# Kernel optimization log

Hardware: AMD Instinct MI355X
Metric: run time of the kernel (lower is better)

The kernel has to match this reference:

```python
import jax, jax.numpy as jnp
import numpy as np

B, H, W, C = 8, 256, 256, 256


def setup_inputs() -> dict:
    key = jax.random.key(0)
    ks = jax.random.split(key, 5)
    scale = 1.0 / np.sqrt(C)
    return {
        "x": jax.random.normal(ks[0], (B, H, W, C), dtype=jnp.float32),
        "wq": jax.random.normal(ks[1], (C, C), dtype=jnp.float32) * scale,
        "bq": jnp.zeros((C,), dtype=jnp.float32),
        "wk": jax.random.normal(ks[2], (C, C), dtype=jnp.float32) * scale,
        "bk": jnp.zeros((C,), dtype=jnp.float32),
        "wv": jax.random.normal(ks[3], (C, C), dtype=jnp.float32) * scale,
        "bv": jnp.zeros((C,), dtype=jnp.float32),
        "gamma": jax.random.normal(ks[4], (C,), dtype=jnp.float32) * scale,
    }


def reference(x, wq, bq, wk, bk, wv, bv, gamma):
    # 1x1 convs == per-pixel channel matmuls
    q = jnp.einsum("bhwc,cd->bhwd", x, wq) + bq  # [B,H,W,C]
    k = jnp.einsum("bhwc,cd->bhwd", x, wk) + bk
    v = jnp.einsum("bhwc,cd->bhwd", x, wv) + bv
    # tf.matmul(q, k, transpose_b=True) on 4D: batch dims (B,H), attention over W
    attn = jax.nn.softmax(jnp.einsum("bhic,bhjc->bhij", q, k), axis=-1)  # [B,H,W,W]
    out = jnp.einsum("bhij,bhjc->bhic", attn, v)  # [B,H,W,C]
    return gamma * out + x
```

## Files before the change

kernel.cpp:

```cpp
#include <hip/hip_runtime.h>


#define NPAIR 2048
#define SEQ 256
#define DIM 256
#define XSTR 264
#define SCRSTR 48

typedef __attribute__((ext_vector_type(8))) short bf16x8;
typedef __attribute__((ext_vector_type(4))) float f32x4;
typedef __attribute__((ext_vector_type(4))) unsigned uint4v;
typedef __attribute__((ext_vector_type(2))) unsigned uint2v;

__device__ __forceinline__ unsigned short f2bf(float f) {
  union { float f; unsigned u; } v; v.f = f;
  unsigned r = v.u + 0x7FFFu + ((v.u >> 16) & 1u);
  return (unsigned short)(r >> 16);
}
__device__ __forceinline__ unsigned pack2(float a, float b) {
  return (unsigned)f2bf(a) | ((unsigned)f2bf(b) << 16);
}

__global__ void prep_kernel(const float* __restrict__ wq, const float* __restrict__ bq,
                            const float* __restrict__ wk, const float* __restrict__ wv,
                            unsigned short* __restrict__ MT, unsigned short* __restrict__ WvT,
                            float* __restrict__ u) {
  int b = blockIdx.x, t = threadIdx.x;
  if (b < 256) {
    int r = b;
    for (int c = t; c < 256; c += blockDim.x) {
      float acc = 0.f;
      for (int d = 0; d < 256; ++d) acc += wq[c * 256 + d] * wk[r * 256 + d];
      MT[r * 256 + c] = f2bf(acc);
    }
  } else if (b == 256) {
    for (int cc = t; cc < 256; cc += blockDim.x) {
      float acc = 0.f;
      for (int d = 0; d < 256; ++d) acc += wk[cc * 256 + d] * bq[d];
      u[cc] = acc;
    }
  } else {
    int r = b - 257;
    for (int c = t; c < 256; c += blockDim.x) WvT[r * 256 + c] = f2bf(wv[c * 256 + r]);
  }
}

__global__ __launch_bounds__(512, 2)
void attn_fused_kernel(const float* __restrict__ x, const unsigned short* __restrict__ MT,
                       const float* __restrict__ u, const unsigned short* __restrict__ WvT,
                       const float* __restrict__ bv, const float* __restrict__ gamma,
                       float* __restrict__ out) {
  __shared__ unsigned short Xs[SEQ * XSTR];
  __shared__ unsigned short Yscr[8][16 * SCRSTR];
  const int p = blockIdx.x;
  const long xbase = (long)p * (SEQ * DIM);
  const int tid = threadIdx.x;
  const int wid = tid >> 6;
  const int ln = tid & 63;
  const int l16 = ln & 15;
  const int quad = ln >> 4;

  for (int it = 0; it < 64; ++it) {
    int idx = 2 * (tid + 512 * it);
    float2 v = *(const float2*)(x + xbase + idx);
    int j = idx >> 8, c = idx & 255;
    unsigned pack = (unsigned)f2bf(v.x) | ((unsigned)f2bf(v.y) << 16);
    *(unsigned*)&Xs[j * XSTR + c] = pack;
  }
  __syncthreads();

  float ureg[16];
#pragma unroll
  for (int nt = 0; nt < 16; ++nt) ureg[nt] = u[nt * 16 + l16];

  unsigned short* Aout =
      (unsigned short*)((char*)out + (size_t)p * (SEQ * DIM * 4) + 131072);
  unsigned short* scr = &Yscr[wid][0];

  for (int ch = 0; ch < 2; ++ch) {
    const int chunk = wid + 8 * ch;
    const int i0 = chunk * 16;

    f32x4 acc[16];
#pragma unroll
    for (int nt = 0; nt < 16; ++nt) acc[nt] = (f32x4){0.f, 0.f, 0.f, 0.f};
#pragma unroll
    for (int ks = 0; ks < 8; ++ks) {
      bf16x8 a = *(const bf16x8*)&Xs[(i0 + l16) * XSTR + ks * 32 + quad * 8];
#pragma unroll
      for (int nt = 0; nt < 16; ++nt) {
        bf16x8 b = *(const bf16x8*)&MT[(nt * 16 + l16) * 256 + ks * 32 + quad * 8];
        acc[nt] = __builtin_amdgcn_mfma_f32_16x16x32_bf16(a, b, acc[nt], 0, 0, 0);
      }
    }

    f32x4 sacc[16];
#pragma unroll
    for (int mt = 0; mt < 16; ++mt) sacc[mt] = (f32x4){0.f, 0.f, 0.f, 0.f};
#pragma unroll
    for (int e = 0; e < 8; ++e) {
      asm volatile("s_waitcnt lgkmcnt(0)" ::: "memory");
#pragma unroll
      for (int h = 0; h < 2; ++h) {
        int nt = 2 * e + h;
#pragma unroll
        for (int r = 0; r < 4; ++r) {
          float yv = acc[nt][r] + ureg[nt];
          scr[(quad * 4 + r) * SCRSTR + h * 16 + l16] = f2bf(yv);
        }
      }
      asm volatile("s_waitcnt lgkmcnt(0)" ::: "memory");
      bf16x8 bfrag = *(const bf16x8*)&scr[l16 * SCRSTR + quad * 8];
#pragma unroll
      for (int mt = 0; mt < 16; ++mt) {
        bf16x8 a = *(const bf16x8*)&Xs[(mt * 16 + l16) * XSTR + e * 32 + quad * 8];
        sacc[mt] = __builtin_amdgcn_mfma_f32_16x16x32_bf16(a, bfrag, sacc[mt], 0, 0, 0);
      }
    }

    float mx = -1e30f;
#pragma unroll
    for (int mt = 0; mt < 16; ++mt)
#pragma unroll
      for (int r = 0; r < 4; ++r) mx = fmaxf(mx, sacc[mt][r]);
    mx = fmaxf(mx, __shfl_xor(mx, 16, 64));
    mx = fmaxf(mx, __shfl_xor(mx, 32, 64));
    float sum = 0.f;
#pragma unroll
    for (int mt = 0; mt < 16; ++mt)
#pragma unroll
      for (int r = 0; r < 4; ++r) {
        float ev = exp2f((sacc[mt][r] - mx) * 1.44269504088896340736f);
        sacc[mt][r] = ev;
        sum += ev;
      }
    sum += __shfl_xor(sum, 16, 64);
    sum += __shfl_xor(sum, 32, 64);
    float rs = 1.0f / sum;

#pragma unroll
    for (int ks = 0; ks < 8; ++ks) {
      asm volatile("s_waitcnt lgkmcnt(0)" ::: "memory");
#pragma unroll
      for (int h = 0; h < 2; ++h) {
        int mt = 2 * ks + h;
        unsigned lo = pack2(sacc[mt][0] * rs, sacc[mt][1] * rs);
        unsigned hi = pack2(sacc[mt][2] * rs, sacc[mt][3] * rs);
        *(unsigned*)&scr[l16 * SCRSTR + h * 16 + quad * 4] = lo;
        *(unsigned*)&scr[l16 * SCRSTR + h * 16 + quad * 4 + 2] = hi;
      }
      asm volatile("s_waitcnt lgkmcnt(0)" ::: "memory");
      uint4v t = *(const uint4v*)&scr[(ln >> 2) * SCRSTR + (ln & 3) * 8];
      *(uint4v*)&Aout[(i0 + (ln >> 2)) * 256 + ks * 32 + (ln & 3) * 8] = t;
    }
  }
  __syncthreads();

  bf16x8 afr[8];
  {
    int i = 16 * wid + l16;
#pragma unroll
    for (int ks = 0; ks < 8; ++ks)
      afr[ks] = *(const bf16x8*)&Aout[i * 256 + ks * 32 + quad * 8];
  }

  unsigned pay[64];
#pragma unroll
  for (int dc = 0; dc < 16; ++dc) {
    bf16x8 bfr[8];
#pragma unroll
    for (int ks = 0; ks < 8; ++ks)
      bfr[ks] = *(const bf16x8*)&WvT[(dc * 16 + l16) * 256 + ks * 32 + quad * 8];
#pragma unroll
    for (int jr = 0; jr < 2; ++jr) {
      const int jc = wid + 8 * jr;
      f32x4 vacc = (f32x4){0.f, 0.f, 0.f, 0.f};
#pragma unroll
      for (int ks = 0; ks < 8; ++ks) {
        bf16x8 a = *(const bf16x8*)&Xs[(jc * 16 + l16) * XSTR + ks * 32 + quad * 8];
        vacc = __builtin_amdgcn_mfma_f32_16x16x32_bf16(a, bfr[ks], vacc, 0, 0, 0);
      }
      pay[dc * 4 + jr * 2 + 0] = pack2(vacc[0], vacc[1]);
      pay[dc * 4 + jr * 2 + 1] = pack2(vacc[2], vacc[3]);
    }
  }
  __syncthreads();
#pragma unroll
  for (int dc = 0; dc < 16; ++dc)
#pragma unroll
    for (int jr = 0; jr < 2; ++jr) {
      const int jc = wid + 8 * jr;
      uint2v w = {pay[dc * 4 + jr * 2], pay[dc * 4 + jr * 2 + 1]};
      *(uint2v*)&Xs[(dc * 16 + l16) * XSTR + jc * 16 + quad * 4] = w;
    }
  float greg[16], bvreg[16];
#pragma unroll
  for (int nt = 0; nt < 16; ++nt) {
    greg[nt] = gamma[nt * 16 + l16];
    bvreg[nt] = bv[nt * 16 + l16];
  }
  __syncthreads();

  float* outp = out + (size_t)p * (SEQ * DIM);
  for (int rnd = 0; rnd < 2; ++rnd) {
    const int i0 = (wid + 8 * rnd) * 16;
    f32x4 oacc[16];
#pragma unroll
    for (int nt = 0; nt < 16; ++nt) oacc[nt] = (f32x4){0.f, 0.f, 0.f, 0.f};
#pragma unroll
    for (int ks = 0; ks < 8; ++ks) {
      bf16x8 a = afr[ks];
#pragma unroll
      for (int nt = 0; nt < 16; ++nt) {
        bf16x8 b = *(const bf16x8*)&Xs[(nt * 16 + l16) * XSTR + ks * 32 + quad * 8];
        oacc[nt] = __builtin_amdgcn_mfma_f32_16x16x32_bf16(a, b, oacc[nt], 0, 0, 0);
      }
    }
    if (rnd == 0) {
      int i = 16 * (8 + wid) + l16;
#pragma unroll
      for (int ks = 0; ks < 8; ++ks)
        afr[ks] = *(const bf16x8*)&Aout[i * 256 + ks * 32 + quad * 8];
      asm volatile("s_waitcnt vmcnt(0)" ::: "memory");
      __syncthreads();
    }
#pragma unroll
    for (int nt = 0; nt < 16; ++nt)
#pragma unroll
      for (int r = 0; r < 4; ++r) {
        int i = i0 + quad * 4 + r;
        int dd = nt * 16 + l16;
        float xv = x[xbase + (long)i * 256 + dd];
        outp[(long)i * 256 + dd] = greg[nt] * (oacc[nt][r] + bvreg[nt]) + xv;
      }
  }
}

extern "C" void kernel_launch(void* const* d_in, const int* in_sizes, int n_in,
                              void* d_out, int out_size, void* d_ws, size_t ws_size,
                              hipStream_t stream) {
  const float* x     = (const float*)d_in[0];
  const float* wq    = (const float*)d_in[1];
  const float* bq    = (const float*)d_in[2];
  const float* wk    = (const float*)d_in[3];
  const float* wv    = (const float*)d_in[5];
  const float* bv    = (const float*)d_in[6];
  const float* gamma = (const float*)d_in[7];
  float* out = (float*)d_out;

  unsigned short* MT  = (unsigned short*)d_ws;
  unsigned short* WvT = MT + 65536;
  float* u            = (float*)(WvT + 65536);

  prep_kernel<<<513, 256, 0, stream>>>(wq, bq, wk, wv, MT, WvT, u);
  attn_fused_kernel<<<NPAIR, 512, 0, stream>>>(x, MT, u, WvT, bv, gamma, out);
}
```

Baseline: 2.457 ms.

## Use 1024-thread blocks with one 16-row chunk per wave, keep attention in registers

The fused kernel now launches 16 waves per block so each wave owns exactly one 16-row query chunk, removing the two-chunk loops. Attention probabilities stay in registers and go through the per-wave scratch into the PV matmul, instead of being written as bf16 to the output buffer in global memory and read back. The V projection is computed per wave for its own rows, and the x load uses float4. The risk is register pressure under launch_bounds(1024,4): the attention values held across the V-projection stage could spill, and with about 143KB of LDS per block occupancy drops to one block per CU.

```diff
diff --git a/kernel.cpp b/kernel.cpp
--- a/kernel.cpp
+++ b/kernel.cpp
@@ -9,7 +9,6 @@
 
 typedef __attribute__((ext_vector_type(8))) short bf16x8;
 typedef __attribute__((ext_vector_type(4))) float f32x4;
-typedef __attribute__((ext_vector_type(4))) unsigned uint4v;
 typedef __attribute__((ext_vector_type(2))) unsigned uint2v;
 
 __device__ __forceinline__ unsigned short f2bf(float f) {
@@ -45,13 +44,13 @@
   }
 }
 
-__global__ __launch_bounds__(512, 2)
+__global__ __launch_bounds__(1024, 4)
 void attn_fused_kernel(const float* __restrict__ x, const unsigned short* __restrict__ MT,
                        const float* __restrict__ u, const unsigned short* __restrict__ WvT,
                        const float* __restrict__ bv, const float* __restrict__ gamma,
                        float* __restrict__ out) {
   __shared__ unsigned short Xs[SEQ * XSTR];
-  __shared__ unsigned short Yscr[8][16 * SCRSTR];
+  __shared__ unsigned short Yscr[16][16 * SCRSTR];
   const int p = blockIdx.x;
   const long xbase = (long)p * (SEQ * DIM);
   const int tid = threadIdx.x;
@@ -59,13 +58,14 @@
   const int ln = tid & 63;
   const int l16 = ln & 15;
   const int quad = ln >> 4;
-
-  for (int it = 0; it < 64; ++it) {
-    int idx = 2 * (tid + 512 * it);
-    float2 v = *(const float2*)(x + xbase + idx);
+  const int i0 = wid * 16;
+
+  for (int it = 0; it < 16; ++it) {
+    int idx = 4 * (tid + 1024 * it);
+    float4 v = *(const float4*)(x + xbase + idx);
     int j = idx >> 8, c = idx & 255;
-    unsigned pack = (unsigned)f2bf(v.x) | ((unsigned)f2bf(v.y) << 16);
-    *(unsigned*)&Xs[j * XSTR + c] = pack;
+    uint2v w = {pack2(v.x, v.y), pack2(v.z, v.w)};
+    *(uint2v*)&Xs[j * XSTR + c] = w;
   }
   __syncthreads();
 
@@ -73,126 +73,95 @@
 #pragma unroll
   for (int nt = 0; nt < 16; ++nt) ureg[nt] = u[nt * 16 + l16];
 
-  unsigned short* Aout =
-      (unsigned short*)((char*)out + (size_t)p * (SEQ * DIM * 4) + 131072);
   unsigned short* scr = &Yscr[wid][0];
 
-  for (int ch = 0; ch < 2; ++ch) {
-    const int chunk = wid + 8 * ch;
-    const int i0 = chunk * 16;
-
-    f32x4 acc[16];
-#pragma unroll
-    for (int nt = 0; nt < 16; ++nt) acc[nt] = (f32x4){0.f, 0.f, 0.f, 0.f};
+  f32x4 acc[16];
+#pragma unroll
+  for (int nt = 0; nt < 16; ++nt) acc[nt] = (f32x4){0.f, 0.f, 0.f, 0.f};
+#pragma unroll
+  for (int ks = 0; ks < 8; ++ks) {
+    bf16x8 a = *(const bf16x8*)&Xs[(i0 + l16) * XSTR + ks * 32 + quad * 8];
+#pragma unroll
+    for (int nt = 0; nt < 16; ++nt) {
+      bf16x8 b = *(const bf16x8*)&MT[(nt * 16 + l16) * 256 + ks * 32 + quad * 8];
+      acc[nt] = __builtin_amdgcn_mfma_f32_16x16x32_bf16(a, b, acc[nt], 0, 0, 0);
+    }
+  }
+
+  f32x4 sacc[16];
+#pragma unroll
+  for (int mt = 0; mt < 16; ++mt) sacc[mt] = (f32x4){0.f, 0.f, 0.f, 0.f};
+#pragma unroll
+  for (int e = 0; e < 8; ++e) {
+    asm volatile("s_waitcnt lgkmcnt(0)" ::: "memory");
+#pragma unroll
+    for (int h = 0; h < 2; ++h) {
+      int nt = 2 * e + h;
+#pragma unroll
+      for (int r = 0; r < 4; ++r) {
+        float yv = acc[nt][r] + ureg[nt];
+        scr[(quad * 4 + r) * SCRSTR + h * 16 + l16] = f2bf(yv);
+      }
+    }
+    asm volatile("s_waitcnt lgkmcnt(0)" ::: "memory");
+    bf16x8 bfrag = *(const bf16x8*)&scr[l16 * SCRSTR + quad * 8];
+#pragma unroll
+    for (int mt = 0; mt < 16; ++mt) {
+      bf16x8 a = *(const bf16x8*)&Xs[(mt * 16 + l16) * XSTR + e * 32 + quad * 8];
+      sacc[mt] = __builtin_amdgcn_mfma_f32_16x16x32_bf16(a, bfrag, sacc[mt], 0, 0, 0);
+    }
+  }
+
+  float mx = -1e30f;
+#pragma unroll
+  for (int mt = 0; mt < 16; ++mt)
+#pragma unroll
+    for (int r = 0; r < 4; ++r) mx = fmaxf(mx, sacc[mt][r]);
+  mx = fmaxf(mx, __shfl_xor(mx, 16, 64));
+  mx = fmaxf(mx, __shfl_xor(mx, 32, 64));
+  float sum = 0.f;
+#pragma unroll
+  for (int mt = 0; mt < 16; ++mt)
+#pragma unroll
+    for (int r = 0; r < 4; ++r) {
+      float ev = exp2f((sacc[mt][r] - mx) * 1.44269504088896340736f);
+      sacc[mt][r] = ev;
+      sum += ev;
+    }
+  sum += __shfl_xor(sum, 16, 64);
+  sum += __shfl_xor(sum, 32, 64);
+  float rs = 1.0f / sum;
+
+  unsigned aw[32];
+#pragma unroll
+  for (int mt = 0; mt < 16; ++mt) {
+    aw[2 * mt]     = pack2(sacc[mt][0] * rs, sacc[mt][1] * rs);
+    aw[2 * mt + 1] = pack2(sacc[mt][2] * rs, sacc[mt][3] * rs);
+  }
+
+  bf16x8 axr[8];
+#pragma unroll
+  for (int ks = 0; ks < 8; ++ks)
+    axr[ks] = *(const bf16x8*)&Xs[(i0 + l16) * XSTR + ks * 32 + quad * 8];
+  unsigned pay[32];
+#pragma unroll
+  for (int dc = 0; dc < 16; ++dc) {
+    f32x4 vacc = (f32x4){0.f, 0.f, 0.f, 0.f};
 #pragma unroll
     for (int ks = 0; ks < 8; ++ks) {
-      bf16x8 a = *(const bf16x8*)&Xs[(i0 + l16) * XSTR + ks * 32 + quad * 8];
-#pragma unroll
-      for (int nt = 0; nt < 16; ++nt) {
-        bf16x8 b = *(const bf16x8*)&MT[(nt * 16 + l16) * 256 + ks * 32 + quad * 8];
-        acc[nt] = __builtin_amdgcn_mfma_f32_16x16x32_bf16(a, b, acc[nt], 0, 0, 0);
-      }
-    }
-
-    f32x4 sacc[16];
-#pragma unroll
-    for (int mt = 0; mt < 16; ++mt) sacc[mt] = (f32x4){0.f, 0.f, 0.f, 0.f};
-#pragma unroll
-    for (int e = 0; e < 8; ++e) {
-      asm volatile("s_waitcnt lgkmcnt(0)" ::: "memory");
-#pragma unroll
-      for (int h = 0; h < 2; ++h) {
-        int nt = 2 * e + h;
-#pragma unroll
-        for (int r = 0; r < 4; ++r) {
-          float yv = acc[nt][r] + ureg[nt];
-          scr[(quad * 4 + r) * SCRSTR + h * 16 + l16] = f2bf(yv);
-        }
-      }
-      asm volatile("s_waitcnt lgkmcnt(0)" ::: "memory");
-      bf16x8 bfrag = *(const bf16x8*)&scr[l16 * SCRSTR + quad * 8];
-#pragma unroll
-      for (int mt = 0; mt < 16; ++mt) {
-        bf16x8 a = *(const bf16x8*)&Xs[(mt * 16 + l16) * XSTR + e * 32 + quad * 8];
-        sacc[mt] = __builtin_amdgcn_mfma_f32_16x16x32_bf16(a, bfrag, sacc[mt], 0, 0, 0);
-      }
-    }
-
-    float mx = -1e30f;
-#pragma unroll
-    for (int mt = 0; mt < 16; ++mt)
-#pragma unroll
-      for (int r = 0; r < 4; ++r) mx = fmaxf(mx, sacc[mt][r]);
-    mx = fmaxf(mx, __shfl_xor(mx, 16, 64));
-    mx = fmaxf(mx, __shfl_xor(mx, 32, 64));
-    float sum = 0.f;
-#pragma unroll
-    for (int mt = 0; mt < 16; ++mt)
-#pragma unroll
-      for (int r = 0; r < 4; ++r) {
-        float ev = exp2f((sacc[mt][r] - mx) * 1.44269504088896340736f);
-        sacc[mt][r] = ev;
-        sum += ev;
-      }
-    sum += __shfl_xor(sum, 16, 64);
-    sum += __shfl_xor(sum, 32, 64);
-    float rs = 1.0f / sum;
-
-#pragma unroll
-    for (int ks = 0; ks < 8; ++ks) {
-      asm volatile("s_waitcnt lgkmcnt(0)" ::: "memory");
-#pragma unroll
-      for (int h = 0; h < 2; ++h) {
-        int mt = 2 * ks + h;
-        unsigned lo = pack2(sacc[mt][0] * rs, sacc[mt][1] * rs);
-        unsigned hi = pack2(sacc[mt][2] * rs, sacc[mt][3] * rs);
-        *(unsigned*)&scr[l16 * SCRSTR + h * 16 + quad * 4] = lo;
-        *(unsigned*)&scr[l16 * SCRSTR + h * 16 + quad * 4 + 2] = hi;
-      }
-      asm volatile("s_waitcnt lgkmcnt(0)" ::: "memory");
-      uint4v t = *(const uint4v*)&scr[(ln >> 2) * SCRSTR + (ln & 3) * 8];
-      *(uint4v*)&Aout[(i0 + (ln >> 2)) * 256 + ks * 32 + (ln & 3) * 8] = t;
-    }
+      bf16x8 b = *(const bf16x8*)&WvT[(dc * 16 + l16) * 256 + ks * 32 + quad * 8];
+      vacc = __builtin_amdgcn_mfma_f32_16x16x32_bf16(axr[ks], b, vacc, 0, 0, 0);
+    }
+    pay[2 * dc]     = pack2(vacc[0], vacc[1]);
+    pay[2 * dc + 1] = pack2(vacc[2], vacc[3]);
   }
   __syncthreads();
 
-  bf16x8 afr[8];
-  {
-    int i = 16 * wid + l16;
-#pragma unroll
-    for (int ks = 0; ks < 8; ++ks)
-      afr[ks] = *(const bf16x8*)&Aout[i * 256 + ks * 32 + quad * 8];
-  }
-
-  unsigned pay[64];
 #pragma unroll
   for (int dc = 0; dc < 16; ++dc) {
-    bf16x8 bfr[8];
-#pragma unroll
-    for (int ks = 0; ks < 8; ++ks)
-      bfr[ks] = *(const bf16x8*)&WvT[(dc * 16 + l16) * 256 + ks * 32 + quad * 8];
-#pragma unroll
-    for (int jr = 0; jr < 2; ++jr) {
-      const int jc = wid + 8 * jr;
-      f32x4 vacc = (f32x4){0.f, 0.f, 0.f, 0.f};
-#pragma unroll
-      for (int ks = 0; ks < 8; ++ks) {
-        bf16x8 a = *(const bf16x8*)&Xs[(jc * 16 + l16) * XSTR + ks * 32 + quad * 8];
-        vacc = __builtin_amdgcn_mfma_f32_16x16x32_bf16(a, bfr[ks], vacc, 0, 0, 0);
-      }
-      pay[dc * 4 + jr * 2 + 0] = pack2(vacc[0], vacc[1]);
-      pay[dc * 4 + jr * 2 + 1] = pack2(vacc[2], vacc[3]);
-    }
-  }
-  __syncthreads();
-#pragma unroll
-  for (int dc = 0; dc < 16; ++dc)
-#pragma unroll
-    for (int jr = 0; jr < 2; ++jr) {
-      const int jc = wid + 8 * jr;
-      uint2v w = {pay[dc * 4 + jr * 2], pay[dc * 4 + jr * 2 + 1]};
-      *(uint2v*)&Xs[(dc * 16 + l16) * XSTR + jc * 16 + quad * 4] = w;
-    }
+    uint2v w = {pay[2 * dc], pay[2 * dc + 1]};
+    *(uint2v*)&Xs[(dc * 16 + l16) * XSTR + i0 + quad * 4] = w;
+  }
   float greg[16], bvreg[16];
 #pragma unroll
   for (int nt = 0; nt < 16; ++nt) {
@@ -201,39 +170,35 @@
   }
   __syncthreads();
 
+  f32x4 oacc[16];
+#pragma unroll
+  for (int nt = 0; nt < 16; ++nt) oacc[nt] = (f32x4){0.f, 0.f, 0.f, 0.f};
+#pragma unroll
+  for (int ks = 0; ks < 8; ++ks) {
+    asm volatile("s_waitcnt lgkmcnt(0)" ::: "memory");
+    uint2v w0 = {aw[4 * ks], aw[4 * ks + 1]};
+    uint2v w1 = {aw[4 * ks + 2], aw[4 * ks + 3]};
+    *(uint2v*)&scr[l16 * SCRSTR + quad * 4] = w0;
+    *(uint2v*)&scr[l16 * SCRSTR + 16 + quad * 4] = w1;
+    asm volatile("s_waitcnt lgkmcnt(0)" ::: "memory");
+    bf16x8 afrag = *(const bf16x8*)&scr[l16 * SCRSTR + quad * 8];
+#pragma unroll
+    for (int nt = 0; nt < 16; ++nt) {
+      bf16x8 b = *(const bf16x8*)&Xs[(nt * 16 + l16) * XSTR + ks * 32 + quad * 8];
+      oacc[nt] = __builtin_amdgcn_mfma_f32_16x16x32_bf16(afrag, b, oacc[nt], 0, 0, 0);
+    }
+  }
+
   float* outp = out + (size_t)p * (SEQ * DIM);
-  for (int rnd = 0; rnd < 2; ++rnd) {
-    const int i0 = (wid + 8 * rnd) * 16;
-    f32x4 oacc[16];
-#pragma unroll
-    for (int nt = 0; nt < 16; ++nt) oacc[nt] = (f32x4){0.f, 0.f, 0.f, 0.f};
-#pragma unroll
-    for (int ks = 0; ks < 8; ++ks) {
-      bf16x8 a = afr[ks];
-#pragma unroll
-      for (int nt = 0; nt < 16; ++nt) {
-        bf16x8 b = *(const bf16x8*)&Xs[(nt * 16 + l16) * XSTR + ks * 32 + quad * 8];
-        oacc[nt] = __builtin_amdgcn_mfma_f32_16x16x32_bf16(a, b, oacc[nt], 0, 0, 0);
-      }
-    }
-    if (rnd == 0) {
-      int i = 16 * (8 + wid) + l16;
-#pragma unroll
-      for (int ks = 0; ks < 8; ++ks)
-        afr[ks] = *(const bf16x8*)&Aout[i * 256 + ks * 32 + quad * 8];
-      asm volatile("s_waitcnt vmcnt(0)" ::: "memory");
-      __syncthreads();
-    }
-#pragma unroll
-    for (int nt = 0; nt < 16; ++nt)
-#pragma unroll
-      for (int r = 0; r < 4; ++r) {
-        int i = i0 + quad * 4 + r;
-        int dd = nt * 16 + l16;
-        float xv = x[xbase + (long)i * 256 + dd];
-        outp[(long)i * 256 + dd] = greg[nt] * (oacc[nt][r] + bvreg[nt]) + xv;
-      }
-  }
+#pragma unroll
+  for (int nt = 0; nt < 16; ++nt)
+#pragma unroll
+    for (int r = 0; r < 4; ++r) {
+      int i = i0 + quad * 4 + r;
+      int dd = nt * 16 + l16;
+      float xv = x[xbase + (long)i * 256 + dd];
+      outp[(long)i * 256 + dd] = greg[nt] * (oacc[nt][r] + bvreg[nt]) + xv;
+    }
 }
 
 extern "C" void kernel_launch(void* const* d_in, const int* in_sizes, int n_in,
@@ -253,5 +218,5 @@
   float* u            = (float*)(WvT + 65536);
 
   prep_kernel<<<513, 256, 0, stream>>>(wq, bq, wk, wv, MT, WvT, u);
-  attn_fused_kernel<<<NPAIR, 512, 0, stream>>>(x, MT, u, WvT, bv, gamma, out);
-}
+  attn_fused_kernel<<<NPAIR, 1024, 0, stream>>>(x, MT, u, WvT, bv, gamma, out);
+}
```

After: 2.237 ms. 1.1x faster.
